# Kernel tuning notes

Hardware: AMD Instinct MI355X
Metric: run time of the kernel (lower is better)

The kernel has to match this reference:

```python
import jax, jax.numpy as jnp
import numpy as np
from jax.scipy.special import i0

IM_SIZE = (256, 256)
GRID_SIZE = (512, 512)
NUMPOINTS = 6
OS = GRID_SIZE[0] / IM_SIZE[0]
# Beatty et al. optimal Kaiser-Bessel shape parameter
BETA = float(np.pi * np.sqrt((NUMPOINTS / OS) ** 2 * (OS - 0.5) ** 2 - 0.8))


def _apod_1d(N, G):
    # 1/FT(kb kernel) scaling coefficients (de-apodization), static numpy
    x = np.arange(N) - N / 2.0
    arg = np.pi * NUMPOINTS * x / G
    t = BETA ** 2 - arg ** 2  # > 0 for this config
    ph = np.sinh(np.sqrt(t)) / np.sqrt(t)
    return (1.0 / ph).astype(np.float32)


def _kb(u):
    # Kaiser-Bessel interpolation kernel, support |u| <= NUMPOINTS/2
    x = 2.0 * u / NUMPOINTS
    t = 1.0 - x * x
    inside = t > 0
    t = jnp.where(inside, t, 0.0)
    return jnp.where(inside, i0(BETA * jnp.sqrt(t)), 0.0)


def setup_inputs():
    key = jax.random.key(0)
    k1, k2, k3 = jax.random.split(key, 3)
    B, M = 8, 131072
    image = jax.random.normal(k1, (B,) + IM_SIZE, dtype=jnp.float32)
    ktraj = (jax.random.uniform(k2, (B, 2, M), dtype=jnp.float32) * 2.0 - 1.0) * jnp.pi
    dcf = jax.random.uniform(k3, (B, M), dtype=jnp.float32)
    return {"image": image, "ktraj": ktraj, "dcf": dcf}


def _nufft(image, ktraj, dcf):
    B = image.shape[0]
    N1, N2 = IM_SIZE
    G1, G2 = GRID_SIZE
    J = NUMPOINTS
    # 1) de-apodization (scaling coefficients), separable per-dim
    a1 = jnp.asarray(_apod_1d(N1, G1))
    a2 = jnp.asarray(_apod_1d(N2, G2))
    img = image.astype(jnp.complex64) * (a1[:, None] * a2[None, :])
    # 2) centered zero-pad to oversampled grid, FFT with DC at bin 0
    p1, p2 = (G1 - N1) // 2, (G2 - N2) // 2
    grid = jnp.zeros((B, G1, G2), dtype=jnp.complex64).at[:, p1:p1 + N1, p2:p2 + N2].set(img)
    kgrid = jnp.fft.fft2(jnp.fft.ifftshift(grid, axes=(1, 2)))
    # 3) KB interpolation (gather) at non-uniform points
    tm1 = ktraj[:, 0] * (G1 / (2.0 * jnp.pi))  # (B,M) in grid units
    tm2 = ktraj[:, 1] * (G2 / (2.0 * jnp.pi))
    offs = jnp.arange(J, dtype=jnp.float32) - (J // 2 - 1)  # [-2..3]
    g1 = jnp.floor(tm1)[..., None] + offs  # (B,M,J) neighbor coords
    g2 = jnp.floor(tm2)[..., None] + offs
    w1 = _kb(tm1[..., None] - g1)
    w2 = _kb(tm2[..., None] - g2)
    i1 = jnp.mod(g1.astype(jnp.int32), G1)
    i2 = jnp.mod(g2.astype(jnp.int32), G2)
    lin = (i1[..., :, None] * G2 + i2[..., None, :]).reshape(B, -1)  # (B, M*J*J)
    vals = jnp.take_along_axis(kgrid.reshape(B, -1), lin, axis=1).reshape(B, -1, J, J)
    w = (w1[..., :, None] * w2[..., None, :]).astype(jnp.complex64)
    kdata = jnp.sum(vals * w, axis=(-1, -2))  # (B,M) complex
    kdata = kdata * dcf
    return jnp.stack([kdata.real, kdata.imag], axis=0)  # (2,B,M) float32


def reference(image, ktraj, dcf):
    return _nufft(image, ktraj, dcf)
```

## Files before the change

kernel.cpp:

```cpp
#include <hip/hip_runtime.h>
#include <math.h>

#define GSZ 512
#define NSZ 256
#define NBATCH 8
#define MPTS 131072
#define PI_F 3.14159265358979f
#define BETA_F 13.8551004f
#define BETA2_F (BETA_F * BETA_F)
#define RSQ2 0.70710678f
#define PADIDX(i) ((i) + ((i) >> 3))

typedef float f32x4 __attribute__((ext_vector_type(4)));


__device__ __forceinline__ float apod(int i) {
    float x = (float)(i - 128);
    float arg = PI_F * 6.0f * x * (1.0f / 512.0f);
    float t = BETA2_F - arg * arg;
    float st = sqrtf(t);
    return 2.0f * st * __expf(-st);
}

__device__ __forceinline__ float kbw(float u) {
    float t = 1.0f - u * u * (1.0f / 9.0f);
    float x = BETA_F * sqrtf(fmaxf(t, 0.0f));
    float xc = fmaxf(x, 0.35f);
    float R = __builtin_amdgcn_rsqf(xc);
    float R2 = R * R;
    float q = R * (0.39894228f + R2 * (0.04986779f + R2 * 0.02804702f));
    float w = __expf(xc) * q;
    return (t > 0.0f) ? w : 0.0f;
}

template<int CTRL>
__device__ __forceinline__ float qdpp(float v) {
    int r = __builtin_amdgcn_mov_dpp(__float_as_int(v), CTRL, 0xF, 0xF, true);
    return __int_as_float(r);
}

__device__ __forceinline__ float2 cadd(float2 a, float2 b){ return make_float2(a.x+b.x, a.y+b.y); }
__device__ __forceinline__ float2 csub(float2 a, float2 b){ return make_float2(a.x-b.x, a.y-b.y); }
__device__ __forceinline__ float2 cmul(float2 a, float2 b){ return make_float2(a.x*b.x-a.y*b.y, a.x*b.y+a.y*b.x); }
__device__ __forceinline__ float2 mul_negi(float2 a){ return make_float2(a.y, -a.x); }
__device__ __forceinline__ float2 mul_posi(float2 a){ return make_float2(-a.y, a.x); }
__device__ __forceinline__ float2 mul_w81(float2 a){ return make_float2(RSQ2*(a.x+a.y), RSQ2*(a.y-a.x)); }
__device__ __forceinline__ float2 mul_w83(float2 a){ return make_float2(RSQ2*(a.y-a.x), -RSQ2*(a.x+a.y)); }

__device__ __forceinline__ void dft8_combine(float2 E0, float2 E1, float2 E2, float2 E3,
                                             float2 O0, float2 O1, float2 O2, float2 O3,
                                             float2* y) {
    float2 c1 = mul_w81(O1), c2 = mul_negi(O2), c3 = mul_w83(O3);
    y[0] = cadd(E0, O0); y[4] = csub(E0, O0);
    y[1] = cadd(E1, c1); y[5] = csub(E1, c1);
    y[2] = cadd(E2, c2); y[6] = csub(E2, c2);
    y[3] = cadd(E3, c3); y[7] = csub(E3, c3);
}

__device__ __forceinline__ void dft8(const float2* x, float2* y) {
    float2 a0=x[0], a1=x[2], a2=x[4], a3=x[6];
    float2 b0=x[1], b1=x[3], b2=x[5], b3=x[7];
    float2 ta0=cadd(a0,a2), ta1=csub(a0,a2), ta2=cadd(a1,a3), ta3=csub(a1,a3);
    float2 E0=cadd(ta0,ta2), E2=csub(ta0,ta2);
    float2 E1=cadd(ta1, mul_negi(ta3)), E3=cadd(ta1, mul_posi(ta3));
    float2 tb0=cadd(b0,b2), tb1=csub(b0,b2), tb2=cadd(b1,b3), tb3=csub(b1,b3);
    float2 O0=cadd(tb0,tb2), O2=csub(tb0,tb2);
    float2 O1=cadd(tb1, mul_negi(tb3)), O3=cadd(tb1, mul_posi(tb3));
    dft8_combine(E0,E1,E2,E3,O0,O1,O2,O3,y);
}

__device__ __forceinline__ void dft8_pruned(float2 x0, float2 x1, float2 x6, float2 x7, float2* y) {
    float2 E0 = cadd(x0, x6), E2 = csub(x0, x6);
    float2 E1 = cadd(x0, mul_posi(x6)), E3 = cadd(x0, mul_negi(x6));
    float2 O0 = cadd(x1, x7), O2 = csub(x1, x7);
    float2 O1 = cadd(x1, mul_posi(x7)), O3 = cadd(x1, mul_negi(x7));
    dft8_combine(E0,E1,E2,E3,O0,O1,O2,O3,y);
}

template<int S>
__device__ __forceinline__ void twiddle8(int t, float2* y) {
    if (S < 2) {
        int j = (S == 0) ? t : (t >> 3);
        const float scale = (S == 0) ? (-2.0f*PI_F/512.0f) : (-2.0f*PI_F/64.0f);
        float theta = scale * (float)j;
        float sn, cs;
        __sincosf(theta, &sn, &cs);
        float2 w = make_float2(cs, sn), wq = w;
        y[1] = cmul(y[1], wq);
        #pragma unroll
        for (int q = 2; q < 8; ++q) { wq = cmul(wq, w); y[q] = cmul(y[q], wq); }
    }
}


__device__ __forceinline__ float2 pswap(float2 v) {
    return make_float2(qdpp<0xB1>(v.x), qdpp<0xB1>(v.y));
}

__device__ __forceinline__ void dft8_half(const float2* v, float2* EO) {
    float2 t0 = cadd(v[0], v[2]), t1 = csub(v[0], v[2]);
    float2 t2 = cadd(v[1], v[3]), t3 = csub(v[1], v[3]);
    EO[0] = cadd(t0, t2); EO[2] = csub(t0, t2);
    EO[1] = cadd(t1, mul_negi(t3)); EO[3] = cadd(t1, mul_posi(t3));
}

__device__ __forceinline__ void dft8p_half(float2 u0, float2 u1, float2* EO) {
    EO[0] = cadd(u0, u1); EO[2] = csub(u0, u1);
    EO[1] = cadd(u0, mul_posi(u1)); EO[3] = cadd(u0, mul_negi(u1));
}

__device__ __forceinline__ void combine_half(int h, const float2* V, float2* y) {
    float2 P0 = pswap(V[0]), P1 = pswap(V[1]), P2 = pswap(V[2]), P3 = pswap(V[3]);
    float2 E0 = h ? P0 : V[0], O0 = h ? V[0] : P0;
    float2 E1 = h ? P1 : V[1], O1 = h ? V[1] : P1;
    float2 E2 = h ? P2 : V[2], O2 = h ? V[2] : P2;
    float2 E3 = h ? P3 : V[3], O3 = h ? V[3] : P3;
    float2 c1 = mul_w81(O1), c2 = mul_negi(O2), c3 = mul_w83(O3);
    float s = h ? -1.0f : 1.0f;
    y[0] = make_float2(fmaf(s, O0.x, E0.x), fmaf(s, O0.y, E0.y));
    y[1] = make_float2(fmaf(s, c1.x, E1.x), fmaf(s, c1.y, E1.y));
    y[2] = make_float2(fmaf(s, c2.x, E2.x), fmaf(s, c2.y, E2.y));
    y[3] = make_float2(fmaf(s, c3.x, E3.x), fmaf(s, c3.y, E3.y));
}

__device__ __forceinline__ void twiddle4h(int jidx, float scale, int h, float2* y) {
    float theta = scale * (float)jidx;
    float sn, cs;
    __sincosf(theta, &sn, &cs);
    float2 w = make_float2(cs, sn);
    float2 w2 = cmul(w, w);
    float2 w4 = cmul(w2, w2);
    float2 m = h ? w4 : make_float2(1.0f, 0.0f);
    y[0] = cmul(y[0], m);
    float2 wq = cmul(m, w); y[1] = cmul(y[1], wq);
    wq = cmul(wq, w);       y[2] = cmul(y[2], wq);
    wq = cmul(wq, w);       y[3] = cmul(y[3], wq);
}

__global__ __launch_bounds__(256) void pass1_rowfft(const float* __restrict__ image,
                                                    float2* __restrict__ T,
                                                    int* __restrict__ cursors) {
    __shared__ float2 sm[2][2][578];
    int tid = threadIdx.x;
    if (blockIdx.x == 0) {
        for (int z = tid; z < 1024; z += 256) cursors[z] = 0;
    }
    int r = tid >> 7;
    int tt = tid & 127;
    int h = tt & 1;
    int b = tt >> 1;
    int blk = blockIdx.x;
    int p = blk & 3;
    int g = blk >> 2;
    int rp = (g << 1) + r;
    int y = (rp < 128) ? rp : (rp + 256);
    int iy = (y < 128) ? (y + 128) : (y - 384);
    float ay = apod(iy);
    const float* irow0 = image + ((size_t)((2 * p)     * NSZ + iy)) * NSZ;
    const float* irow1 = image + ((size_t)((2 * p + 1) * NSZ + iy)) * NSZ;

    float2 y4[4];
    {
        int iA = h ? (b + 192) : (b + 128);
        int iB = h ? (b + 64)  : b;
        float wA = ay * apod(iA), wB = ay * apod(iB);
        float2 u0 = make_float2(irow0[iA] * wA, irow1[iA] * wA);
        float2 u1 = make_float2(irow0[iB] * wB, irow1[iB] * wB);
        float2 EO[4];
        dft8p_half(u0, u1, EO);
        combine_half(h, EO, y4);
        twiddle4h(b, -2.0f * PI_F / 512.0f, h, y4);
    }
    float2* A  = sm[0][r];
    float2* Bf = sm[1][r];
    #pragma unroll
    for (int qq = 0; qq < 4; ++qq) A[PADIDX((b << 3) + (h << 2) + qq)] = y4[qq];
    __syncthreads();
    {
        float2 v[4];
        #pragma unroll
        for (int i = 0; i < 4; ++i) v[i] = A[PADIDX(b + (((i << 1) + h) << 6))];
        float2 EO[4];
        dft8_half(v, EO);
        combine_half(h, EO, y4);
        twiddle4h(b >> 3, -2.0f * PI_F / 64.0f, h, y4);
        int base = (b & 7) + ((b >> 3) << 6);
        #pragma unroll
        for (int qq = 0; qq < 4; ++qq) Bf[PADIDX(base + (((h << 2) + qq) << 3))] = y4[qq];
    }
    __syncthreads();
    {
        float2 v[4];
        #pragma unroll
        for (int i = 0; i < 4; ++i) v[i] = Bf[PADIDX(b + (((i << 1) + h) << 6))];
        float2 EO[4];
        dft8_half(v, EO);
        combine_half(h, EO, y4);
        float2* Trow = T + (((size_t)(p << 8) + rp) << 9);
        #pragma unroll
        for (int qq = 0; qq < 4; ++qq) Trow[b + (((h << 2) + qq) << 6)] = y4[qq];
    }
}

__global__ __launch_bounds__(256) void pass2_colfft(const float2* __restrict__ T,
                                                    float2* __restrict__ kgrid,
                                                    const float* __restrict__ ktraj,
                                                    const float* __restrict__ dcf,
                                                    int* __restrict__ cursors,
                                                    float4* __restrict__ sortedpt) {
    __shared__ float4 smemBuf[4224];
    int tid = threadIdx.x;
    int blk = blockIdx.x;

    if (blk >= 256) {
        int u = blk - 256;
        int bs = u >> 5, seg = u & 31;
        const float SCALE = (float)GSZ / (2.0f * PI_F);
        const float* kt1 = ktraj + (size_t)(bs * 2) * MPTS;
        const float* kt2 = kt1 + MPTS;
        const float* dcfb = dcf + ((size_t)bs << 17);
        int* cur = cursors + (bs << 7);
        float4* sp = sortedpt + ((size_t)bs << 18);

        float4* pts = smemBuf;
        int* hist = (int*)(smemBuf + 4096);
        int* lofs = hist + 128;
        int* gbase = hist + 256;
        int* lcur = hist + 384;

        if (tid < 128) hist[tid] = 0;
        __syncthreads();

        float t1v[16], t2v[16], dv[16];
        #pragma unroll
        for (int k = 0; k < 16; ++k) {
            int m = (seg << 12) + (k << 8) + tid;
            t1v[k] = kt1[m] * SCALE;
            t2v[k] = kt2[m] * SCALE;
            dv[k]  = dcfb[m];
            int key = (((int)floorf(t1v[k])) & 511) >> 2;
            atomicAdd(&hist[key], 1);
        }
        __syncthreads();

        if (tid == 0) {
            int s = 0;
            #pragma unroll 8
            for (int i = 0; i < 128; ++i) { lofs[i] = s; s += hist[i]; }
        }
        if (tid < 128) { gbase[tid] = atomicAdd(cur + tid, hist[tid]); lcur[tid] = 0; }
        __syncthreads();

        #pragma unroll
        for (int k = 0; k < 16; ++k) {
            int m = (seg << 12) + (k << 8) + tid;
            int key = (((int)floorf(t1v[k])) & 511) >> 2;
            int loc = atomicAdd(&lcur[key], 1);
            pts[lofs[key] + loc] =
                make_float4(t1v[k], t2v[k], dv[k], __int_as_float((key << 17) | m));
        }
        __syncthreads();

        #pragma unroll
        for (int k = 0; k < 16; ++k) {
            int s = (k << 8) + tid;
            float4 p = pts[s];
            int w = __float_as_int(p.w);
            int key = w >> 17;
            int m = w & 0x1FFFF;
            int gpos = gbase[key] + (s - lofs[key]);
            if (gpos < 2048)
                sp[((size_t)key << 11) + gpos] =
                    make_float4(p.x, p.y, p.z, __int_as_float(m));
        }
        return;
    }

    float2 (*B)[578] = reinterpret_cast<float2(*)[578]>(smemBuf);
    int p = blk & 3;
    int g = blk >> 2;
    const float2* Tb = T + ((size_t)p << 17);
    float2* Kb0 = kgrid + ((size_t)(2 * p) << 18);
    float2* Kb1 = Kb0 + ((size_t)1 << 18);

    #define COLG(c) ((g > 0) ? (((c) < 4) ? ((g << 2) + (c)) : (505 - (g << 2) + (c))) \
                             : (((c) < 4) ? (c) : (((c) == 7) ? 256 : (505 + (c)))))

    {
        int c = tid & 7, r0 = tid >> 3;
        int colg = COLG(c);
        #pragma unroll
        for (int k = 0; k < 8; ++k) {
            int rr = r0 + (k << 5);
            B[c][PADIDX(rr)] = Tb[((size_t)rr << 9) + colg];
        }
    }
    __syncthreads();
    int t = tid & 63;
    int c0 = tid >> 6;
    float2* Ba = B[c0];
    float2* Bb = B[c0 + 4];
    float2 ya[8], yb[8];
    {
        float2 a0 = Ba[PADIDX(t)],       a1 = Ba[PADIDX(t + 64)];
        float2 a6 = Ba[PADIDX(t + 128)], a7 = Ba[PADIDX(t + 192)];
        float2 b0 = Bb[PADIDX(t)],       b1 = Bb[PADIDX(t + 64)];
        float2 b6 = Bb[PADIDX(t + 128)], b7 = Bb[PADIDX(t + 192)];
        dft8_pruned(a0, a1, a6, a7, ya); twiddle8<0>(t, ya);
        dft8_pruned(b0, b1, b6, b7, yb); twiddle8<0>(t, yb);
    }
    __syncthreads();
    #pragma unroll
    for (int q = 0; q < 8; ++q) {
        Ba[PADIDX((t << 3) + q)] = ya[q];
        Bb[PADIDX((t << 3) + q)] = yb[q];
    }
    __syncthreads();
    {
        float2 xa[8], xb[8];
        #pragma unroll
        for (int pp = 0; pp < 8; ++pp) { xa[pp] = Ba[PADIDX(t + (pp << 6))]; xb[pp] = Bb[PADIDX(t + (pp << 6))]; }
        dft8(xa, ya); twiddle8<1>(t, ya);
        dft8(xb, yb); twiddle8<1>(t, yb);
    }
    __syncthreads();
    {
        int j = t >> 3, k = t & 7, base = k + (j << 6);
        #pragma unroll
        for (int q = 0; q < 8; ++q) {
            Ba[PADIDX(base + (q << 3))] = ya[q];
            Bb[PADIDX(base + (q << 3))] = yb[q];
        }
    }
    __syncthreads();
    {
        float2 xa[8], xb[8];
        #pragma unroll
        for (int pp = 0; pp < 8; ++pp) { xa[pp] = Ba[PADIDX(t + (pp << 6))]; xb[pp] = Bb[PADIDX(t + (pp << 6))]; }
        dft8(xa, ya);
        dft8(xb, yb);
    }
    __syncthreads();
    #pragma unroll
    for (int q = 0; q < 8; ++q) {
        Ba[PADIDX(t + (q << 6))] = ya[q];
        Bb[PADIDX(t + (q << 6))] = yb[q];
    }
    __syncthreads();
    {
        int c = tid & 7, r0 = tid >> 3;
        int colg = COLG(c);
        int mc = 7 - c;
        if (g == 0) { if (c == 0) mc = 0; else if (c == 7) mc = 7; }
        #pragma unroll
        for (int k = 0; k < 16; ++k) {
            int rr = r0 + (k << 5);
            int mr = (512 - rr) & 511;
            float2 Z = B[c][PADIDX(rr)];
            float2 M = B[mc][PADIDX(mr)];
            float2 K0 = make_float2(0.5f * (Z.x + M.x), 0.5f * (Z.y - M.y));
            float2 K1 = make_float2(0.5f * (Z.y + M.y), 0.5f * (M.x - Z.x));
            size_t off = ((size_t)rr << 9) + colg;
            Kb0[off] = K0;
            Kb1[off] = K1;
        }
    }
    #undef COLG
}

__global__ __launch_bounds__(256) void interp_kb(const float2* __restrict__ kgrid,
                                                 const int* __restrict__ cursors,
                                                 const float4* __restrict__ sortedpt,
                                                 float* __restrict__ out) {
    __shared__ float lds[9 * 1028];
    int tid = threadIdx.x;
    int blk = blockIdx.x;
    int b = blk & 7;
    int band = blk >> 3;
    int j = tid & 3;
    int q = tid >> 2;
    int j2 = j << 1;
    float fjm2 = (float)(j - 2), fjp2 = (float)(j + 2);

    int cnt = cursors[(b << 7) + band];
    cnt = (cnt > 2048) ? 2048 : cnt;
    if (cnt == 0) return;

    const float2* Kb = kgrid + ((size_t)b << 18);
    #pragma unroll
    for (int r = 0; r < 9; ++r) {
        int gr = ((band << 2) - 2 + r) & 511;
        const float4* src = (const float4*)(Kb + ((size_t)gr << 9));
        *(float4*)(lds + r * 1028 + (tid << 2)) = src[tid];
    }
    __syncthreads();

    const float4* sp = sortedpt + ((size_t)b << 18) + ((size_t)band << 11);
    float* out_re = out + ((size_t)b << 17);
    float* out_im = out_re + (size_t)NBATCH * MPTS;

    int iters = (cnt + 63) >> 6;
    for (int it = 0; it < iters; ++it) {
        int pidx = (it << 6) + q;
        bool valid = pidx < cnt;
        float4 pt = sp[valid ? pidx : 0];
        float tm1 = pt.x, tm2 = pt.y, dd = pt.z;
        int m = __float_as_int(pt.w);

        float f1 = floorf(tm1), f2 = floorf(tm2);
        int if1 = (int)f1, if2 = (int)f2;
        int e0 = (if2 - 2) & ~1;
        int cpair = (e0 + j2) & 511;
        int lr = (if1 & 511) - (band << 2);

        float u2 = tm2 - (float)(e0 + j2);
        float w2a = kbw(u2);
        float w2b = kbw(u2 - 1.0f);
        float fr1 = tm1 - f1;
        float w1A = kbw(fr1 - fjm2);
        float w1B = kbw(fr1 - fjp2);
        float w0_ = qdpp<0x00>(w1A);
        float w1_ = qdpp<0x55>(w1A);
        float w2_ = qdpp<0xAA>(w1A);
        float w3_ = qdpp<0xFF>(w1A);
        float w4_ = qdpp<0x00>(w1B);
        float w5_ = qdpp<0x55>(w1B);

        const float* lp = lds + (cpair << 1);
        f32x4 v0 = *(const f32x4*)(lp + (lr + 0) * 1028);
        f32x4 v1 = *(const f32x4*)(lp + (lr + 1) * 1028);
        f32x4 v2 = *(const f32x4*)(lp + (lr + 2) * 1028);
        f32x4 v3 = *(const f32x4*)(lp + (lr + 3) * 1028);
        f32x4 v4 = *(const f32x4*)(lp + (lr + 4) * 1028);
        f32x4 v5 = *(const f32x4*)(lp + (lr + 5) * 1028);

        float c0re = w0_ * v0.x, c0im = w0_ * v0.y;
        float c1re = w0_ * v0.z, c1im = w0_ * v0.w;
        c0re = fmaf(w1_, v1.x, c0re); c0im = fmaf(w1_, v1.y, c0im);
        c1re = fmaf(w1_, v1.z, c1re); c1im = fmaf(w1_, v1.w, c1im);
        c0re = fmaf(w2_, v2.x, c0re); c0im = fmaf(w2_, v2.y, c0im);
        c1re = fmaf(w2_, v2.z, c1re); c1im = fmaf(w2_, v2.w, c1im);
        c0re = fmaf(w3_, v3.x, c0re); c0im = fmaf(w3_, v3.y, c0im);
        c1re = fmaf(w3_, v3.z, c1re); c1im = fmaf(w3_, v3.w, c1im);
        c0re = fmaf(w4_, v4.x, c0re); c0im = fmaf(w4_, v4.y, c0im);
        c1re = fmaf(w4_, v4.z, c1re); c1im = fmaf(w4_, v4.w, c1im);
        c0re = fmaf(w5_, v5.x, c0re); c0im = fmaf(w5_, v5.y, c0im);
        c1re = fmaf(w5_, v5.z, c1re); c1im = fmaf(w5_, v5.w, c1im);
        float p_re = fmaf(w2a, c0re, w2b * c1re);
        float p_im = fmaf(w2a, c0im, w2b * c1im);
        p_re += qdpp<0xB1>(p_re); p_re += qdpp<0x4E>(p_re);
        p_im += qdpp<0xB1>(p_im); p_im += qdpp<0x4E>(p_im);

        if (valid) {
            if (j == 0) out_re[m] = p_re * dd;
            else if (j == 1) out_im[m] = p_im * dd;
        }
    }
}


extern "C" void kernel_launch(void* const* d_in, const int* in_sizes, int n_in,
                              void* d_out, int out_size, void* d_ws, size_t ws_size,
                              hipStream_t stream) {
    const float* image = (const float*)d_in[0];
    const float* ktraj = (const float*)d_in[1];
    const float* dcf   = (const float*)d_in[2];
    float* out = (float*)d_out;

    float2* T        = (float2*)d_ws;
    float2* kgrid    = T + (size_t)4 * 256 * GSZ;
    int*    cursors  = (int*)((char*)d_ws + 20971520);
    float4* sortedpt = (float4*)((char*)d_ws + 20975616);

    pass1_rowfft<<<512, 256, 0, stream>>>(image, T, cursors);
    pass2_colfft<<<512, 256, 0, stream>>>(T, kgrid, ktraj, dcf, cursors, sortedpt);
    interp_kb<<<1024, 256, 0, stream>>>(kgrid, cursors, sortedpt, out);
}
```

Before: 123.3 us.

## Store k-space grid transposed and bin points by second coordinate

The column-FFT pass now writes the oversampled k-space grid transposed (column-major), so each column is contiguous. Points are bucketed by their second trajectory coordinate instead of the first. The interpolation kernel loads 9 contiguous columns into LDS and swaps the roles of the two axes in the weight and gather code. The likely aim is contiguous output writes from the column FFT, which previously wrote strided 8-byte elements per row. The trade-off is that writes are now strided along the other index inside the FFT pass.

```diff
diff --git a/kernel.cpp b/kernel.cpp
--- a/kernel.cpp
+++ b/kernel.cpp
@@ -203,7 +203,7 @@
 }
 
 __global__ __launch_bounds__(256) void pass2_colfft(const float2* __restrict__ T,
-                                                    float2* __restrict__ kgrid,
+                                                    float2* __restrict__ kgridT,
                                                     const float* __restrict__ ktraj,
                                                     const float* __restrict__ dcf,
                                                     int* __restrict__ cursors,
@@ -238,7 +238,7 @@
             t1v[k] = kt1[m] * SCALE;
             t2v[k] = kt2[m] * SCALE;
             dv[k]  = dcfb[m];
-            int key = (((int)floorf(t1v[k])) & 511) >> 2;
+            int key = (((int)floorf(t2v[k])) & 511) >> 2;
             atomicAdd(&hist[key], 1);
         }
         __syncthreads();
@@ -254,7 +254,7 @@
         #pragma unroll
         for (int k = 0; k < 16; ++k) {
             int m = (seg << 12) + (k << 8) + tid;
-            int key = (((int)floorf(t1v[k])) & 511) >> 2;
+            int key = (((int)floorf(t2v[k])) & 511) >> 2;
             int loc = atomicAdd(&lcur[key], 1);
             pts[lofs[key] + loc] =
                 make_float4(t1v[k], t2v[k], dv[k], __int_as_float((key << 17) | m));
@@ -280,7 +280,7 @@
     int p = blk & 3;
     int g = blk >> 2;
     const float2* Tb = T + ((size_t)p << 17);
-    float2* Kb0 = kgrid + ((size_t)(2 * p) << 18);
+    float2* Kb0 = kgridT + ((size_t)(2 * p) << 18);
     float2* Kb1 = Kb0 + ((size_t)1 << 18);
 
     #define COLG(c) ((g > 0) ? (((c) < 4) ? ((g << 2) + (c)) : (505 - (g << 2) + (c))) \
@@ -360,7 +360,7 @@
             float2 M = B[mc][PADIDX(mr)];
             float2 K0 = make_float2(0.5f * (Z.x + M.x), 0.5f * (Z.y - M.y));
             float2 K1 = make_float2(0.5f * (Z.y + M.y), 0.5f * (M.x - Z.x));
-            size_t off = ((size_t)rr << 9) + colg;
+            size_t off = ((size_t)colg << 9) + rr;
             Kb0[off] = K0;
             Kb1[off] = K1;
         }
@@ -368,7 +368,7 @@
     #undef COLG
 }
 
-__global__ __launch_bounds__(256) void interp_kb(const float2* __restrict__ kgrid,
+__global__ __launch_bounds__(256) void interp_kb(const float2* __restrict__ kgridT,
                                                  const int* __restrict__ cursors,
                                                  const float4* __restrict__ sortedpt,
                                                  float* __restrict__ out) {
@@ -386,11 +386,11 @@
     cnt = (cnt > 2048) ? 2048 : cnt;
     if (cnt == 0) return;
 
-    const float2* Kb = kgrid + ((size_t)b << 18);
+    const float2* Kb = kgridT + ((size_t)b << 18);
     #pragma unroll
     for (int r = 0; r < 9; ++r) {
-        int gr = ((band << 2) - 2 + r) & 511;
-        const float4* src = (const float4*)(Kb + ((size_t)gr << 9));
+        int gc = ((band << 2) - 2 + r) & 511;
+        const float4* src = (const float4*)(Kb + ((size_t)gc << 9));
         *(float4*)(lds + r * 1028 + (tid << 2)) = src[tid];
     }
     __syncthreads();
@@ -409,30 +409,30 @@
 
         float f1 = floorf(tm1), f2 = floorf(tm2);
         int if1 = (int)f1, if2 = (int)f2;
-        int e0 = (if2 - 2) & ~1;
-        int cpair = (e0 + j2) & 511;
-        int lr = (if1 & 511) - (band << 2);
-
-        float u2 = tm2 - (float)(e0 + j2);
-        float w2a = kbw(u2);
-        float w2b = kbw(u2 - 1.0f);
-        float fr1 = tm1 - f1;
-        float w1A = kbw(fr1 - fjm2);
-        float w1B = kbw(fr1 - fjp2);
-        float w0_ = qdpp<0x00>(w1A);
-        float w1_ = qdpp<0x55>(w1A);
-        float w2_ = qdpp<0xAA>(w1A);
-        float w3_ = qdpp<0xFF>(w1A);
-        float w4_ = qdpp<0x00>(w1B);
-        float w5_ = qdpp<0x55>(w1B);
-
-        const float* lp = lds + (cpair << 1);
-        f32x4 v0 = *(const f32x4*)(lp + (lr + 0) * 1028);
-        f32x4 v1 = *(const f32x4*)(lp + (lr + 1) * 1028);
-        f32x4 v2 = *(const f32x4*)(lp + (lr + 2) * 1028);
-        f32x4 v3 = *(const f32x4*)(lp + (lr + 3) * 1028);
-        f32x4 v4 = *(const f32x4*)(lp + (lr + 4) * 1028);
-        f32x4 v5 = *(const f32x4*)(lp + (lr + 5) * 1028);
+        int e1 = (if1 - 2) & ~1;
+        int rpair = (e1 + j2) & 511;
+        int csoff = (if2 & 511) - (band << 2);
+
+        float u1 = tm1 - (float)(e1 + j2);
+        float wra = kbw(u1);
+        float wrb = kbw(u1 - 1.0f);
+        float fr2 = tm2 - f2;
+        float wA = kbw(fr2 - fjm2);
+        float wB = kbw(fr2 - fjp2);
+        float w0_ = qdpp<0x00>(wA);
+        float w1_ = qdpp<0x55>(wA);
+        float w2_ = qdpp<0xAA>(wA);
+        float w3_ = qdpp<0xFF>(wA);
+        float w4_ = qdpp<0x00>(wB);
+        float w5_ = qdpp<0x55>(wB);
+
+        const float* lp = lds + (rpair << 1) + csoff * 1028;
+        f32x4 v0 = *(const f32x4*)(lp + 0 * 1028);
+        f32x4 v1 = *(const f32x4*)(lp + 1 * 1028);
+        f32x4 v2 = *(const f32x4*)(lp + 2 * 1028);
+        f32x4 v3 = *(const f32x4*)(lp + 3 * 1028);
+        f32x4 v4 = *(const f32x4*)(lp + 4 * 1028);
+        f32x4 v5 = *(const f32x4*)(lp + 5 * 1028);
 
         float c0re = w0_ * v0.x, c0im = w0_ * v0.y;
         float c1re = w0_ * v0.z, c1im = w0_ * v0.w;
@@ -446,8 +446,8 @@
         c1re = fmaf(w4_, v4.z, c1re); c1im = fmaf(w4_, v4.w, c1im);
         c0re = fmaf(w5_, v5.x, c0re); c0im = fmaf(w5_, v5.y, c0im);
         c1re = fmaf(w5_, v5.z, c1re); c1im = fmaf(w5_, v5.w, c1im);
-        float p_re = fmaf(w2a, c0re, w2b * c1re);
-        float p_im = fmaf(w2a, c0im, w2b * c1im);
+        float p_re = fmaf(wra, c0re, wrb * c1re);
+        float p_im = fmaf(wra, c0im, wrb * c1im);
         p_re += qdpp<0xB1>(p_re); p_re += qdpp<0x4E>(p_re);
         p_im += qdpp<0xB1>(p_im); p_im += qdpp<0x4E>(p_im);
 
@@ -468,11 +468,11 @@
     float* out = (float*)d_out;
 
     float2* T        = (float2*)d_ws;
-    float2* kgrid    = T + (size_t)4 * 256 * GSZ;
+    float2* kgridT   = T + (size_t)4 * 256 * GSZ;
     int*    cursors  = (int*)((char*)d_ws + 20971520);
     float4* sortedpt = (float4*)((char*)d_ws + 20975616);
 
     pass1_rowfft<<<512, 256, 0, stream>>>(image, T, cursors);
-    pass2_colfft<<<512, 256, 0, stream>>>(T, kgrid, ktraj, dcf, cursors, sortedpt);
-    interp_kb<<<1024, 256, 0, stream>>>(kgrid, cursors, sortedpt, out);
-}
+    pass2_colfft<<<512, 256, 0, stream>>>(T, kgridT, ktraj, dcf, cursors, sortedpt);
+    interp_kb<<<1024, 256, 0, stream>>>(kgridT, cursors, sortedpt, out);
+}
```

Result: no change. 121.2 us (-1.7%).
